# Performance work log

Hardware: AMD Instinct MI355X
Metric: run time of the kernel (lower is better)

The kernel has to match this reference:

```python
import jax, jax.numpy as jnp
import numpy as np


def _block_diag_linear(x, w, b):
    # x: [B, L, D]; w: [H, bw, bw]; b: [H, bw]
    B, L, D = x.shape
    H, bw, _ = w.shape
    xb = x.reshape(B, L, H, bw)
    y = jnp.einsum('blhi,hij->blhj', xb, w) + b
    return y.reshape(B, L, D)


def setup_inputs() -> dict:
    key = jax.random.key(0)
    ks = jax.random.split(key, 6)
    B, L, D, H = 4, 4096, 2048, 8
    bw = D // H
    std = float(np.sqrt(1.0 / bw))
    x = jax.random.normal(ks[0], (B, L, D), dtype=jnp.float32)
    hidden_state = jnp.zeros((B, D), dtype=jnp.float32)
    # a_param init: exp(-8*sigmoid(a)*softplus(a)) uniform on [0.9, 0.999]
    unif = jax.random.uniform(ks[1], (D,), dtype=jnp.float32)
    min_rad, max_rad = 0.9, 0.999
    a_real = 0.5 * jnp.log(unif * (max_rad**2 - min_rad**2) + min_rad**2 + 1e-08)
    a_param = jnp.log(jnp.exp(-a_real) - 1.0)
    ig_w = std * jax.random.normal(ks[2], (H, bw, bw), dtype=jnp.float32)
    ig_b = jnp.zeros((H, bw), dtype=jnp.float32)
    ag_w = std * jax.random.normal(ks[3], (H, bw, bw), dtype=jnp.float32)
    ag_b = jnp.zeros((H, bw), dtype=jnp.float32)
    return {"x": x, "hidden_state": hidden_state, "a_param": a_param,
            "ig_w": ig_w, "ig_b": ig_b, "ag_w": ag_w, "ag_b": ag_b}


def reference(x, hidden_state, a_param, ig_w, ig_b, ag_w, ag_b):
    # x: [B, L, D]
    gate_x = jax.nn.sigmoid(_block_diag_linear(x, ig_w, ig_b))
    gate_a = jax.nn.sigmoid(_block_diag_linear(x, ag_w, ag_b))
    log_a = -8.0 * gate_a * jax.nn.softplus(a_param)          # [B, L, D]
    a = jnp.exp(log_a)
    multiplier = jnp.sqrt(jnp.clip(1.0 - jnp.exp(2.0 * log_a), 0.0))
    normalized_x = x * gate_x * multiplier                    # [B, L, D]

    def step(h, inp):
        a_t, x_t = inp
        h = a_t * h + x_t
        return h, h

    # scan over time: move L to leading axis
    a_t = jnp.swapaxes(a, 0, 1)               # [L, B, D]
    nx_t = jnp.swapaxes(normalized_x, 0, 1)   # [L, B, D]
    h_final, ys = jax.lax.scan(step, hidden_state, (a_t, nx_t))
    y = jnp.swapaxes(ys, 0, 1)                # [B, L, D]
    return y, h_final
```

## Files before the change

### kernel.cpp

```cpp
#include <hip/hip_runtime.h>
#include <hip/hip_bf16.h>

#define BB 4
#define LL 4096
#define DD 2048
#define HH 8
#define NC 64
#define LC (LL/NC)

typedef __attribute__((ext_vector_type(8))) short short8;
typedef __attribute__((ext_vector_type(4))) float f32x4;
typedef __attribute__((ext_vector_type(2))) float f32x2;

__device__ __forceinline__ float sigmf(float z) { return 1.0f / (1.0f + __expf(-z)); }

__global__ void k_cvt_x(const float* __restrict__ x, short* __restrict__ xb) {
    int i = blockIdx.x * blockDim.x + threadIdx.x;
    int base = i * 8;
    float4 v0 = *reinterpret_cast<const float4*>(x + base);
    float4 v1 = *reinterpret_cast<const float4*>(x + base + 4);
    float tmp[8] = {v0.x, v0.y, v0.z, v0.w, v1.x, v1.y, v1.z, v1.w};
    short8 o;
    #pragma unroll
    for (int j = 0; j < 8; ++j) {
        __hip_bfloat16 b = __float2bfloat16(tmp[j]);
        o[j] = *reinterpret_cast<short*>(&b);
    }
    *reinterpret_cast<short8*>(xb + base) = o;
}

__global__ void k_cvt_w(const float* __restrict__ igw, const float* __restrict__ agw,
                        short* __restrict__ wt) {
    int t = blockIdx.x * blockDim.x + threadIdx.x;
    int g = t >> 19;
    int r = t & 524287;
    int h = r >> 16;
    int j = (r >> 8) & 255;
    int i = r & 255;
    const float* src = (g == 0) ? igw : agw;
    float v = src[(h << 16) + (i << 8) + j];
    __hip_bfloat16 b = __float2bfloat16(v);
    wt[t] = *reinterpret_cast<short*>(&b);
}

__global__ void k_msp(const float* __restrict__ ap, float* __restrict__ msp) {
    int d = blockIdx.x * blockDim.x + threadIdx.x;
    float v = ap[d];
    float sp = (v > 20.f) ? v : log1pf(expf(v));
    msp[d] = -8.0f * sp;
}

__launch_bounds__(256, 2)
__global__ void k_gates(const short* __restrict__ xb, const short* __restrict__ wt,
                        const float* __restrict__ x, const float* __restrict__ msp,
                        const float* __restrict__ igb, const float* __restrict__ agb,
                        float* __restrict__ aout, float* __restrict__ nxout) {
    __shared__ __align__(16) short As[128 * 64];
    __shared__ __align__(16) short Bs[2][128 * 64];

    const int tid  = threadIdx.x;
    const int lane = tid & 63;
    const int w    = tid >> 6;
    const int wr   = w >> 1, wc = w & 1;
    const int mBase = blockIdx.x * 128;
    const int nBase = blockIdx.y * 128;
    const int h     = blockIdx.z;

    f32x4 acc[2][4][4];
    #pragma unroll
    for (int g = 0; g < 2; ++g)
        #pragma unroll
        for (int m = 0; m < 4; ++m)
            #pragma unroll
            for (int n = 0; n < 4; ++n)
                acc[g][m][n] = (f32x4){0.f, 0.f, 0.f, 0.f};

    for (int ks = 0; ks < 4; ++ks) {
        const int kBase = ks * 64;
        __syncthreads();
        #pragma unroll
        for (int i = 0; i < 4; ++i) {
            int cid = tid + (i << 8);
            int r = cid >> 3, c = cid & 7;
            short8 v = *reinterpret_cast<const short8*>(
                xb + (mBase + r) * 2048 + (h << 8) + kBase + (c << 3));
            *reinterpret_cast<short8*>(&As[(r << 6) + (((c ^ (r & 7))) << 3)]) = v;
        }
        #pragma unroll
        for (int g = 0; g < 2; ++g) {
            #pragma unroll
            for (int i = 0; i < 4; ++i) {
                int cid = tid + (i << 8);
                int r = cid >> 3, c = cid & 7;
                short8 v = *reinterpret_cast<const short8*>(
                    wt + ((((g << 3) + h) << 8) + nBase + r) * 256 + kBase + (c << 3));
                *reinterpret_cast<short8*>(&Bs[g][(r << 6) + (((c ^ (r & 7))) << 3)]) = v;
            }
        }
        __syncthreads();
        #pragma unroll
        for (int kk = 0; kk < 2; ++kk) {
            short8 af[4];
            #pragma unroll
            for (int m = 0; m < 4; ++m) {
                int ro = wr * 64 + m * 16 + (lane & 15);
                int ch = ((kk << 2) + (lane >> 4)) ^ (ro & 7);
                af[m] = *reinterpret_cast<const short8*>(&As[(ro << 6) + (ch << 3)]);
            }
            #pragma unroll
            for (int g = 0; g < 2; ++g) {
                #pragma unroll
                for (int n = 0; n < 4; ++n) {
                    int no = wc * 64 + n * 16 + (lane & 15);
                    int ch = ((kk << 2) + (lane >> 4)) ^ (no & 7);
                    short8 bf = *reinterpret_cast<const short8*>(&Bs[g][(no << 6) + (ch << 3)]);
                    #pragma unroll
                    for (int m = 0; m < 4; ++m) {
                        acc[g][m][n] = __builtin_amdgcn_mfma_f32_16x16x32_bf16(
                            af[m], bf, acc[g][m][n], 0, 0, 0);
                    }
                }
            }
        }
    }

    const int r4 = lane >> 4;
    const int cl = lane & 15;
    #pragma unroll
    for (int m = 0; m < 4; ++m) {
        #pragma unroll
        for (int n = 0; n < 4; ++n) {
            int jc   = nBase + wc * 64 + n * 16 + cl;
            int dcol = (h << 8) + jc;
            float bi = igb[dcol];
            float ba = agb[dcol];
            float ms = msp[dcol];
            #pragma unroll
            for (int r = 0; r < 4; ++r) {
                int p = mBase + wr * 64 + m * 16 + r4 * 4 + r;
                float zi = acc[0][m][n][r] + bi;
                float za = acc[1][m][n][r] + ba;
                float gx = sigmf(zi);
                float ga = sigmf(za);
                float la = ms * ga;
                float av = __expf(la);
                float mult = sqrtf(fmaxf(1.0f - av * av, 0.0f));
                int idx = p * 2048 + dcol;
                float xv = x[idx];
                aout[idx]  = av;
                nxout[idx] = xv * gx * mult;
            }
        }
    }
}

__global__ void k_scanA(const float* __restrict__ aD, const float* __restrict__ nxD,
                        float* __restrict__ P, float* __restrict__ S) {
    int d2 = blockIdx.x * blockDim.x + threadIdx.x;
    int c = blockIdx.y, b = blockIdx.z;
    int base = ((b << 12) + c * LC) * 2048 + (d2 << 1);
    float h0 = 0.f, h1 = 0.f, p0 = 1.f, p1 = 1.f;
    #pragma unroll 8
    for (int s = 0; s < LC; ++s) {
        f32x2 av = *reinterpret_cast<const f32x2*>(aD  + base + s * 2048);
        f32x2 nv = *reinterpret_cast<const f32x2*>(nxD + base + s * 2048);
        h0 = fmaf(av[0], h0, nv[0]);
        h1 = fmaf(av[1], h1, nv[1]);
        p0 *= av[0];
        p1 *= av[1];
    }
    int o = ((b * NC + c) << 11) + (d2 << 1);
    f32x2 pp; pp[0] = p0; pp[1] = p1;
    f32x2 ss; ss[0] = h0; ss[1] = h1;
    *reinterpret_cast<f32x2*>(P + o) = pp;
    *reinterpret_cast<f32x2*>(S + o) = ss;
}

__global__ void k_mid(const float* __restrict__ hs, const float* __restrict__ P,
                      const float* __restrict__ S, float* __restrict__ H0) {
    int t = blockIdx.x * blockDim.x + threadIdx.x;
    int b = t >> 11, d = t & 2047;
    float h = hs[t];
    for (int c = 0; c < NC; ++c) {
        int o = ((b * NC + c) << 11) + d;
        H0[o] = h;
        h = fmaf(P[o], h, S[o]);
    }
}

__global__ void k_scanB(const float* aD, const float* __restrict__ nxD,
                        const float* __restrict__ H0, float* y, float* __restrict__ hf) {
    int d2 = blockIdx.x * blockDim.x + threadIdx.x;
    int c = blockIdx.y, b = blockIdx.z;
    int base = ((b << 12) + c * LC) * 2048 + (d2 << 1);
    int o = ((b * NC + c) << 11) + (d2 << 1);
    f32x2 h = *reinterpret_cast<const f32x2*>(H0 + o);
    float h0 = h[0], h1 = h[1];
    #pragma unroll 8
    for (int s = 0; s < LC; ++s) {
        f32x2 av = *reinterpret_cast<const f32x2*>(aD  + base + s * 2048);
        f32x2 nv = *reinterpret_cast<const f32x2*>(nxD + base + s * 2048);
        h0 = fmaf(av[0], h0, nv[0]);
        h1 = fmaf(av[1], h1, nv[1]);
        f32x2 oo; oo[0] = h0; oo[1] = h1;
        *reinterpret_cast<f32x2*>(y + base + s * 2048) = oo;
    }
    if (c == NC - 1) {
        f32x2 oo; oo[0] = h0; oo[1] = h1;
        *reinterpret_cast<f32x2*>(hf + (b << 11) + (d2 << 1)) = oo;
    }
}

extern "C" void kernel_launch(void* const* d_in, const int* in_sizes, int n_in,
                              void* d_out, int out_size, void* d_ws, size_t ws_size,
                              hipStream_t stream) {
    (void)in_sizes; (void)n_in; (void)out_size; (void)ws_size;
    const float* x   = (const float*)d_in[0];
    const float* hs  = (const float*)d_in[1];
    const float* ap  = (const float*)d_in[2];
    const float* igw = (const float*)d_in[3];
    const float* igb = (const float*)d_in[4];
    const float* agw = (const float*)d_in[5];
    const float* agb = (const float*)d_in[6];

    float* y  = (float*)d_out;
    float* hf = y + 33554432;

    char*  ws  = (char*)d_ws;
    short* xb  = (short*)(ws);
    short* wt  = (short*)(ws + 67108864);
    float* msp = (float*)(ws + 69206016);
    float* nx  = (float*)(ws + 69214208);
    float* P   = (float*)(ws + 203431936);
    float* S   = (float*)(ws + 205529088);
    float* H0  = (float*)(ws + 207626240);
    float* aD  = y;

    k_cvt_x<<<16384, 256, 0, stream>>>(x, xb);
    k_cvt_w<<<4096, 256, 0, stream>>>(igw, agw, wt);
    k_msp<<<8, 256, 0, stream>>>(ap, msp);
    k_gates<<<dim3(128, 2, 8), 256, 0, stream>>>(xb, wt, x, msp, igb, agb, aD, nx);
    k_scanA<<<dim3(4, NC, BB), 256, 0, stream>>>(aD, nx, P, S);
    k_mid<<<32, 256, 0, stream>>>(hs, P, S, H0);
    k_scanB<<<dim3(4, NC, BB), 256, 0, stream>>>(aD, nx, H0, y, hf);
}
```

Measured before the change: 533.2 us.

## Fuse x conversion and chunk scan into gate GEMM, pack a/nx as bf16

Removes the separate x-to-bf16 conversion kernel by converting fp32 x while loading the GEMM A tile. Moves the per-chunk prefix (product of a and local scan sum) into the gate GEMM epilogue using wave shuffles, which eliminates the scanA pass. Stores log2(a) and normalized x as two bf16 halves in a single 32-bit word, halving intermediate traffic for scanB, which recomputes a with exp2. The cost is reduced precision for both a and nx, plus extra conversion work inside the GEMM loads.

```diff
diff --git a/kernel.cpp b/kernel.cpp
--- a/kernel.cpp
+++ b/kernel.cpp
@@ -11,22 +11,16 @@
 typedef __attribute__((ext_vector_type(8))) short short8;
 typedef __attribute__((ext_vector_type(4))) float f32x4;
 typedef __attribute__((ext_vector_type(2))) float f32x2;
+typedef __attribute__((ext_vector_type(2))) unsigned int u32x2;
 
 __device__ __forceinline__ float sigmf(float z) { return 1.0f / (1.0f + __expf(-z)); }
 
-__global__ void k_cvt_x(const float* __restrict__ x, short* __restrict__ xb) {
-    int i = blockIdx.x * blockDim.x + threadIdx.x;
-    int base = i * 8;
-    float4 v0 = *reinterpret_cast<const float4*>(x + base);
-    float4 v1 = *reinterpret_cast<const float4*>(x + base + 4);
-    float tmp[8] = {v0.x, v0.y, v0.z, v0.w, v1.x, v1.y, v1.z, v1.w};
-    short8 o;
-    #pragma unroll
-    for (int j = 0; j < 8; ++j) {
-        __hip_bfloat16 b = __float2bfloat16(tmp[j]);
-        o[j] = *reinterpret_cast<short*>(&b);
-    }
-    *reinterpret_cast<short8*>(xb + base) = o;
+__device__ __forceinline__ unsigned short bf16bits(float v) {
+    __hip_bfloat16 b = __float2bfloat16(v);
+    return *reinterpret_cast<unsigned short*>(&b);
+}
+__device__ __forceinline__ float bitsf(unsigned int u) {
+    return *reinterpret_cast<float*>(&u);
 }
 
 __global__ void k_cvt_w(const float* __restrict__ igw, const float* __restrict__ agw,
@@ -39,22 +33,22 @@
     int i = r & 255;
     const float* src = (g == 0) ? igw : agw;
     float v = src[(h << 16) + (i << 8) + j];
-    __hip_bfloat16 b = __float2bfloat16(v);
-    wt[t] = *reinterpret_cast<short*>(&b);
-}
-
-__global__ void k_msp(const float* __restrict__ ap, float* __restrict__ msp) {
+    wt[t] = (short)bf16bits(v);
+}
+
+__global__ void k_msp(const float* __restrict__ ap, float* __restrict__ msp2) {
     int d = blockIdx.x * blockDim.x + threadIdx.x;
     float v = ap[d];
     float sp = (v > 20.f) ? v : log1pf(expf(v));
-    msp[d] = -8.0f * sp;
+    msp2[d] = -8.0f * sp * 1.44269504088896f;
 }
 
 __launch_bounds__(256, 2)
-__global__ void k_gates(const short* __restrict__ xb, const short* __restrict__ wt,
-                        const float* __restrict__ x, const float* __restrict__ msp,
+__global__ void k_gates(const float* __restrict__ x, const short* __restrict__ wt,
+                        const float* __restrict__ msp2,
                         const float* __restrict__ igb, const float* __restrict__ agb,
-                        float* __restrict__ aout, float* __restrict__ nxout) {
+                        unsigned int* __restrict__ packed,
+                        float* __restrict__ P, float* __restrict__ S) {
     __shared__ __align__(16) short As[128 * 64];
     __shared__ __align__(16) short Bs[2][128 * 64];
 
@@ -82,9 +76,15 @@
         for (int i = 0; i < 4; ++i) {
             int cid = tid + (i << 8);
             int r = cid >> 3, c = cid & 7;
-            short8 v = *reinterpret_cast<const short8*>(
-                xb + (mBase + r) * 2048 + (h << 8) + kBase + (c << 3));
-            *reinterpret_cast<short8*>(&As[(r << 6) + (((c ^ (r & 7))) << 3)]) = v;
+            const float* src = x + (mBase + r) * 2048 + (h << 8) + kBase + (c << 3);
+            float4 v0 = *reinterpret_cast<const float4*>(src);
+            float4 v1 = *reinterpret_cast<const float4*>(src + 4);
+            short8 o;
+            o[0] = (short)bf16bits(v0.x); o[1] = (short)bf16bits(v0.y);
+            o[2] = (short)bf16bits(v0.z); o[3] = (short)bf16bits(v0.w);
+            o[4] = (short)bf16bits(v1.x); o[5] = (short)bf16bits(v1.y);
+            o[6] = (short)bf16bits(v1.z); o[7] = (short)bf16bits(v1.w);
+            *reinterpret_cast<short8*>(&As[(r << 6) + ((c ^ (r & 7)) << 3)]) = o;
         }
         #pragma unroll
         for (int g = 0; g < 2; ++g) {
@@ -94,7 +94,7 @@
                 int r = cid >> 3, c = cid & 7;
                 short8 v = *reinterpret_cast<const short8*>(
                     wt + ((((g << 3) + h) << 8) + nBase + r) * 256 + kBase + (c << 3));
-                *reinterpret_cast<short8*>(&Bs[g][(r << 6) + (((c ^ (r & 7))) << 3)]) = v;
+                *reinterpret_cast<short8*>(&Bs[g][(r << 6) + ((c ^ (r & 7)) << 3)]) = v;
             }
         }
         __syncthreads();
@@ -126,54 +126,59 @@
 
     const int r4 = lane >> 4;
     const int cl = lane & 15;
+    const int cg = blockIdx.x * 2 + wr;
+
     #pragma unroll
-    for (int m = 0; m < 4; ++m) {
-        #pragma unroll
-        for (int n = 0; n < 4; ++n) {
-            int jc   = nBase + wc * 64 + n * 16 + cl;
-            int dcol = (h << 8) + jc;
-            float bi = igb[dcol];
-            float ba = agb[dcol];
-            float ms = msp[dcol];
+    for (int n = 0; n < 4; ++n) {
+        int dcol = (h << 8) + nBase + wc * 64 + n * 16 + cl;
+        float bi  = igb[dcol];
+        float ba  = agb[dcol];
+        float ms2 = msp2[dcol];
+        float Am[4], Sm[4];
+        #pragma unroll
+        for (int m = 0; m < 4; ++m) {
+            float Ar = 1.f, Sr = 0.f;
             #pragma unroll
             for (int r = 0; r < 4; ++r) {
-                int p = mBase + wr * 64 + m * 16 + r4 * 4 + r;
                 float zi = acc[0][m][n][r] + bi;
                 float za = acc[1][m][n][r] + ba;
                 float gx = sigmf(zi);
                 float ga = sigmf(za);
-                float la = ms * ga;
-                float av = __expf(la);
-                float mult = sqrtf(fmaxf(1.0f - av * av, 0.0f));
-                int idx = p * 2048 + dcol;
-                float xv = x[idx];
-                aout[idx]  = av;
-                nxout[idx] = xv * gx * mult;
-            }
-        }
-    }
-}
-
-__global__ void k_scanA(const float* __restrict__ aD, const float* __restrict__ nxD,
-                        float* __restrict__ P, float* __restrict__ S) {
-    int d2 = blockIdx.x * blockDim.x + threadIdx.x;
-    int c = blockIdx.y, b = blockIdx.z;
-    int base = ((b << 12) + c * LC) * 2048 + (d2 << 1);
-    float h0 = 0.f, h1 = 0.f, p0 = 1.f, p1 = 1.f;
-    #pragma unroll 8
-    for (int s = 0; s < LC; ++s) {
-        f32x2 av = *reinterpret_cast<const f32x2*>(aD  + base + s * 2048);
-        f32x2 nv = *reinterpret_cast<const f32x2*>(nxD + base + s * 2048);
-        h0 = fmaf(av[0], h0, nv[0]);
-        h1 = fmaf(av[1], h1, nv[1]);
-        p0 *= av[0];
-        p1 *= av[1];
-    }
-    int o = ((b * NC + c) << 11) + (d2 << 1);
-    f32x2 pp; pp[0] = p0; pp[1] = p1;
-    f32x2 ss; ss[0] = h0; ss[1] = h1;
-    *reinterpret_cast<f32x2*>(P + o) = pp;
-    *reinterpret_cast<f32x2*>(S + o) = ss;
+                float la2 = ms2 * ga;
+                unsigned int labits = ((unsigned int)bf16bits(la2)) << 16;
+                float a = exp2f(bitsf(labits));
+                float mult = sqrtf(fmaxf(1.0f - a * a, 0.0f));
+                int p = mBase + wr * 64 + m * 16 + r4 * 4 + r;
+                float xv = x[p * 2048 + dcol];
+                float nx = xv * gx * mult;
+                unsigned short nxb = bf16bits(nx);
+                packed[p * 2048 + dcol] = labits | (unsigned int)nxb;
+                float nxr = bitsf(((unsigned int)nxb) << 16);
+                Sr = fmaf(a, Sr, nxr);
+                Ar *= a;
+            }
+            Am[m] = Ar; Sm[m] = Sr;
+        }
+        #pragma unroll
+        for (int st = 0; st < 2; ++st) {
+            int msk = 16 << st;
+            #pragma unroll
+            for (int m = 0; m < 4; ++m) {
+                float Ap = __shfl_xor(Am[m], msk, 64);
+                float Sp = __shfl_xor(Sm[m], msk, 64);
+                if (lane & msk) Sm[m] = fmaf(Am[m], Sp, Sm[m]);
+                else            Sm[m] = fmaf(Ap, Sm[m], Sp);
+                Am[m] *= Ap;
+            }
+        }
+        float Ac = Am[0], Sc = Sm[0];
+        #pragma unroll
+        for (int m = 1; m < 4; ++m) { Sc = fmaf(Am[m], Sc, Sm[m]); Ac *= Am[m]; }
+        if (r4 == 0) {
+            P[cg * 2048 + dcol] = Ac;
+            S[cg * 2048 + dcol] = Sc;
+        }
+    }
 }
 
 __global__ void k_mid(const float* __restrict__ hs, const float* __restrict__ P,
@@ -188,8 +193,9 @@
     }
 }
 
-__global__ void k_scanB(const float* aD, const float* __restrict__ nxD,
-                        const float* __restrict__ H0, float* y, float* __restrict__ hf) {
+__global__ void k_scanB(const unsigned int* __restrict__ pk,
+                        const float* __restrict__ H0,
+                        float* __restrict__ y, float* __restrict__ hf) {
     int d2 = blockIdx.x * blockDim.x + threadIdx.x;
     int c = blockIdx.y, b = blockIdx.z;
     int base = ((b << 12) + c * LC) * 2048 + (d2 << 1);
@@ -198,10 +204,13 @@
     float h0 = h[0], h1 = h[1];
     #pragma unroll 8
     for (int s = 0; s < LC; ++s) {
-        f32x2 av = *reinterpret_cast<const f32x2*>(aD  + base + s * 2048);
-        f32x2 nv = *reinterpret_cast<const f32x2*>(nxD + base + s * 2048);
-        h0 = fmaf(av[0], h0, nv[0]);
-        h1 = fmaf(av[1], h1, nv[1]);
+        u32x2 wv = *reinterpret_cast<const u32x2*>(pk + base + s * 2048);
+        float a0  = exp2f(bitsf(wv[0] & 0xFFFF0000u));
+        float nx0 = bitsf(wv[0] << 16);
+        float a1  = exp2f(bitsf(wv[1] & 0xFFFF0000u));
+        float nx1 = bitsf(wv[1] << 16);
+        h0 = fmaf(a0, h0, nx0);
+        h1 = fmaf(a1, h1, nx1);
         f32x2 oo; oo[0] = h0; oo[1] = h1;
         *reinterpret_cast<f32x2*>(y + base + s * 2048) = oo;
     }
@@ -226,21 +235,17 @@
     float* y  = (float*)d_out;
     float* hf = y + 33554432;
 
-    char*  ws  = (char*)d_ws;
-    short* xb  = (short*)(ws);
-    short* wt  = (short*)(ws + 67108864);
-    float* msp = (float*)(ws + 69206016);
-    float* nx  = (float*)(ws + 69214208);
-    float* P   = (float*)(ws + 203431936);
-    float* S   = (float*)(ws + 205529088);
-    float* H0  = (float*)(ws + 207626240);
-    float* aD  = y;
-
-    k_cvt_x<<<16384, 256, 0, stream>>>(x, xb);
+    char*         ws   = (char*)d_ws;
+    short*        wt   = (short*)(ws);
+    float*        msp2 = (float*)(ws + 2097152);
+    unsigned int* pk   = (unsigned int*)(ws + 2105344);
+    float*        P    = (float*)(ws + 136323072);
+    float*        S    = (float*)(ws + 138420224);
+    float*        H0   = (float*)(ws + 140517376);
+
     k_cvt_w<<<4096, 256, 0, stream>>>(igw, agw, wt);
-    k_msp<<<8, 256, 0, stream>>>(ap, msp);
-    k_gates<<<dim3(128, 2, 8), 256, 0, stream>>>(xb, wt, x, msp, igb, agb, aD, nx);
-    k_scanA<<<dim3(4, NC, BB), 256, 0, stream>>>(aD, nx, P, S);
+    k_msp<<<8, 256, 0, stream>>>(ap, msp2);
+    k_gates<<<dim3(128, 2, 8), 256, 0, stream>>>(x, wt, msp2, igb, agb, pk, P, S);
     k_mid<<<32, 256, 0, stream>>>(hs, P, S, H0);
-    k_scanB<<<dim3(4, NC, BB), 256, 0, stream>>>(aD, nx, H0, y, hf);
-}
+    k_scanB<<<dim3(4, NC, BB), 256, 0, stream>>>(pk, H0, y, hf);
+}
```

Result: faster. 448.1 us (-16.0%).
